# Performance work log

Hardware: AMD Instinct MI355X
Metric: run time of the kernel (lower is better)

## Reference

```python
import jax, jax.numpy as jnp
import numpy as np

H = 256; NL = 6; N = 64; DCONV = 4; DIN = 512; HEADS = 8; P = 64
CONVD = DIN + 2 * N            # 640
PROJ = 2 * DIN + 2 * N + HEADS  # 1160


def rmsnorm(x, w, eps=1e-6):
    return x * jax.lax.rsqrt(jnp.mean(x * x, axis=-1, keepdims=True) + eps) * w


def mamba2(x, Win, conv_w, conv_b, dt_bias, A_log, D, gnorm, Wout):
    # x: (b, l, H)
    b, l, _ = x.shape
    zxbcdt = x @ Win                       # (b, l, PROJ)
    z = zxbcdt[..., :DIN]
    xBC = zxbcdt[..., DIN:DIN + CONVD]
    dt = zxbcdt[..., DIN + CONVD:]         # (b, l, HEADS)
    # causal depthwise conv1d along l
    xp = jnp.pad(xBC, ((0, 0), (DCONV - 1, 0), (0, 0)))
    xc = conv_b + sum(xp[:, k:k + l, :] * conv_w[k] for k in range(DCONV))
    xBC = jax.nn.silu(xc)
    xs = xBC[..., :DIN]
    B = xBC[..., DIN:DIN + N]
    C = xBC[..., DIN + N:]
    dt = jax.nn.softplus(dt + dt_bias)
    dA = jnp.exp(dt * (-jnp.exp(A_log)))   # (b, l, HEADS)
    xh = xs.reshape(b, l, HEADS, P)
    xdt = xh * dt[..., None]

    def step(h, inp):
        dA_t, xdt_t, B_t, C_t = inp
        h = dA_t[:, :, None, None] * h + xdt_t[..., None] * B_t[:, None, None, :]
        return h, jnp.einsum('bhpn,bn->bhp', h, C_t)

    h0 = jnp.zeros((b, HEADS, P, N), x.dtype)
    _, ys = jax.lax.scan(step, h0, (jnp.swapaxes(dA, 0, 1), jnp.swapaxes(xdt, 0, 1),
                                    jnp.swapaxes(B, 0, 1), jnp.swapaxes(C, 0, 1)))
    y = jnp.swapaxes(ys, 0, 1) + D[None, None, :, None] * xh   # (b, l, HEADS, P)
    y = y.reshape(b, l, DIN) * jax.nn.silu(z)
    return rmsnorm(y, gnorm) @ Wout


def dual_path(x, t_norm, t_Win, t_cw, t_cb, t_dtb, t_Alog, t_D, t_gn, t_Wout,
              b_norm, b_Win, b_cw, b_cb, b_dtb, b_Alog, b_D, b_gn, b_Wout):
    batch, time, bands, hdim = x.shape
    for i in range(NL):
        # time-axis pass (raw row-major reshape, matching torch .reshape semantics)
        xt = x.reshape(batch * bands, time, hdim)
        xt = xt + mamba2(rmsnorm(xt, t_norm[i]), t_Win[i], t_cw[i], t_cb[i],
                         t_dtb[i], t_Alog[i], t_D[i], t_gn[i], t_Wout[i])
        x = jnp.swapaxes(xt.reshape(batch, bands, time, hdim), 1, 2)
        # band-axis pass
        xb = x.reshape(batch * time, bands, hdim)
        xb = xb + mamba2(rmsnorm(xb, b_norm[i]), b_Win[i], b_cw[i], b_cb[i],
                         b_dtb[i], b_Alog[i], b_D[i], b_gn[i], b_Wout[i])
        x = xb.reshape(batch, time, bands, hdim)
    return x


def setup_inputs() -> dict:
    key = jax.random.key(0)
    ks = jax.random.split(key, 3)
    x = jax.random.normal(ks[0], (2, 512, 64, H), jnp.float32)

    def make_params(k):
        kk = jax.random.split(k, 5)
        g = lambda kx, sh, s: jax.random.normal(kx, sh, jnp.float32) * s
        return dict(
            norm=jnp.ones((NL, H), jnp.float32),
            Win=g(kk[0], (NL, H, PROJ), H ** -0.5),
            cw=g(kk[1], (NL, DCONV, CONVD), 0.2),
            cb=jnp.zeros((NL, CONVD), jnp.float32),
            dtb=g(kk[2], (NL, HEADS), 0.5),
            Alog=jnp.log(jnp.abs(g(kk[3], (NL, HEADS), 1.0)) + 0.5),
            D=jnp.ones((NL, HEADS), jnp.float32),
            gn=jnp.ones((NL, DIN), jnp.float32),
            Wout=g(kk[4], (NL, DIN, H), DIN ** -0.5),
        )

    tp = make_params(ks[1]); bp = make_params(ks[2])
    out = {'x': x}
    for name, d in (('t', tp), ('b', bp)):
        for kname, v in d.items():
            out[f'{name}_{kname}'] = v
    return out


def reference(x, t_norm, t_Win, t_cw, t_cb, t_dtb, t_Alog, t_D, t_gn, t_Wout,
              b_norm, b_Win, b_cw, b_cb, b_dtb, b_Alog, b_D, b_gn, b_Wout):
    return dual_path(x, t_norm, t_Win, t_cw, t_cb, t_dtb, t_Alog, t_D, t_gn, t_Wout,
                     b_norm, b_Win, b_cw, b_cb, b_dtb, b_Alog, b_D, b_gn, b_Wout)
```

## Files before the change

### kernel.cpp

```cpp
#include <hip/hip_runtime.h>
#include <math.h>

#define NLAY   6
#define Hd     256
#define DINv   512
#define NHEADS 8
#define CONVDv 640
#define PROJv  1160
#define ZW     656
#define NTOK   65536
#define NCH    1024

typedef __attribute__((ext_vector_type(8))) short bf16x8;
typedef __attribute__((ext_vector_type(4))) float f32x4;
typedef unsigned short u16;

__device__ __forceinline__ float siluf(float v) { return v / (1.0f + expf(-v)); }
__device__ __forceinline__ float bflo(unsigned u) { return __uint_as_float(u << 16); }
__device__ __forceinline__ float bfhi(unsigned u) { return __uint_as_float(u & 0xffff0000u); }
__device__ __forceinline__ u16 f2b(float f) {
    unsigned u = __float_as_uint(f);
    return (u16)((u + 0x7fffu + ((u >> 16) & 1u)) >> 16);
}
__device__ __forceinline__ float b2f(u16 s) { return __uint_as_float(((unsigned)s) << 16); }

__device__ __forceinline__ void gl_lds16(const void* g, void* l) {
    __builtin_amdgcn_global_load_lds((const __attribute__((address_space(1))) unsigned int*)g,
                                     (__attribute__((address_space(3))) unsigned int*)l, 16, 0, 0);
}

__global__ __launch_bounds__(512)
void kprep_win(const float* __restrict__ tW, const float* __restrict__ bW,
               u16* __restrict__ Whi, u16* __restrict__ Wlo)
{
    const int li = blockIdx.y, j = blockIdx.x;
    const int t  = threadIdx.x;
    const int kk = t >> 6, col = (t >> 2) & 15, quad = t & 3;
    const float* W = (li < 6) ? (tW + (size_t)li * Hd * PROJv)
                              : (bW + (size_t)(li - 6) * Hd * PROJv);
    const int fullcol = 16 * j + col;
    const size_t ob = ((size_t)li * 74 + j) * 4096 + kk * 512 + col * 32 + quad * 8;
#pragma unroll
    for (int e = 0; e < 8; e++) {
        const int k = kk * 32 + quad * 8 + e;
        const float v = (fullcol < PROJv) ? W[(size_t)k * PROJv + fullcol] : 0.f;
        const u16 hi = f2b(v);
        Whi[ob + e] = hi;
        Wlo[ob + e] = f2b(v - b2f(hi));
    }
}

__global__ __launch_bounds__(512)
void kprep_wout(const float* __restrict__ tW, const float* __restrict__ tg,
                const float* __restrict__ bW, const float* __restrict__ bg,
                u16* __restrict__ Whi, u16* __restrict__ Wlo)
{
    const int li = blockIdx.y, j = blockIdx.x;
    const int t  = threadIdx.x;
    const int kk = t >> 5, col = (t >> 1) & 15, qh = t & 1;
    const float* W = (li < 6) ? tW + (size_t)li * DINv * Hd : bW + (size_t)(li - 6) * DINv * Hd;
    const float* g = (li < 6) ? tg + li * DINv : bg + (li - 6) * DINv;
    const int fullcol = 16 * j + col;
#pragma unroll
    for (int q = 0; q < 2; q++) {
        const int quad = qh * 2 + q;
        const size_t ob = ((size_t)li * 16 + j) * 8192 + kk * 512 + col * 32 + quad * 8;
#pragma unroll
        for (int e = 0; e < 8; e++) {
            const int k = kk * 32 + quad * 8 + e;
            const float v = W[(size_t)k * Hd + fullcol] * g[k];
            const u16 hi = f2b(v);
            Whi[ob + e] = hi;
            Wlo[ob + e] = f2b(v - b2f(hi));
        }
    }
}

__global__ __launch_bounds__(512, 4)
void k1_mfma(const float* __restrict__ src, u16* __restrict__ zs,
             u16* __restrict__ xrawT, u16* __restrict__ bnd,
             const float* __restrict__ nw,
             const u16* __restrict__ Whi, const u16* __restrict__ Wlo)
{
    __shared__ __align__(16) char smem[67584];
    u16* sAh = (u16*)smem;
    u16* sAl = sAh + 64 * 264;
    const int tid = threadIdx.x;
    const int cb  = blockIdx.x;
    const int R0  = cb * 64;

    {
        const int tok = tid >> 3, l8 = tid & 7;
        const float* xr = src + ((size_t)(R0 + tok)) * Hd + l8 * 32;
        float vv[32];
#pragma unroll
        for (int q = 0; q < 8; q++) {
            float4 v = ((const float4*)xr)[q];
            vv[4*q] = v.x; vv[4*q+1] = v.y; vv[4*q+2] = v.z; vv[4*q+3] = v.w;
        }
        float ss = 0.f;
#pragma unroll
        for (int j = 0; j < 32; j++) ss += vv[j] * vv[j];
#pragma unroll
        for (int m = 4; m >= 1; m >>= 1) ss += __shfl_xor(ss, m, 8);
        const float rstd = rsqrtf(ss * (1.0f / Hd) + 1e-6f);
        const float* nr = nw + l8 * 32;
        u16* dh = sAh + tok * 264 + l8 * 32;
        u16* dl = sAl + tok * 264 + l8 * 32;
#pragma unroll
        for (int j = 0; j < 32; j++) {
            const float val = vv[j] * rstd * nr[j];
            const u16 hi = f2b(val);
            dh[j] = hi;
            dl[j] = f2b(val - b2f(hi));
        }
    }
    __syncthreads();

    const int lane = tid & 63, wave = tid >> 6;
    const int rh = wave >> 1, cw = wave & 1;
    const int quad = lane >> 4, m16 = lane & 15;

    bf16x8 ah[8], al[8];
    {
        const u16* ph = sAh + (rh * 16 + m16) * 264 + quad * 8;
        const u16* pl = sAl + (rh * 16 + m16) * 264 + quad * 8;
#pragma unroll
        for (int kk = 0; kk < 8; kk++) {
            ah[kk] = *(const bf16x8*)(ph + kk * 32);
            al[kk] = *(const bf16x8*)(pl + kk * 32);
        }
    }
    __syncthreads();

    u16* sW = (u16*)smem;

#define K1_STAGE(p, buf)                                                          \
    {                                                                             \
        const int obase = wave * 4096;                                            \
        _Pragma("unroll")                                                         \
        for (int i = 0; i < 4; i++) {                                             \
            const int o = obase + i * 1024;                                       \
            const int chunk = o >> 13, t2 = chunk >> 1, hl = chunk & 1;           \
            const int within = o & 8191;                                          \
            const u16* sbase = (hl ? Wlo : Whi) + (size_t)(2 * (p) + t2) * 4096;  \
            gl_lds16((const char*)sbase + within + lane * 16,                     \
                     (char*)sW + (buf) * 32768 + o);                              \
        }                                                                         \
    }

    K1_STAGE(0, 0);
    __syncthreads();

    for (int p = 0; p < 37; p++) {
        if (p < 36) K1_STAGE(p + 1, (p + 1) & 1);
        const int j = 2 * p + cw;
        const u16* tb = sW + (p & 1) * 16384 + cw * 8192 + m16 * 32 + quad * 8;
        f32x4 acc = (f32x4){0.f, 0.f, 0.f, 0.f};
#pragma unroll
        for (int kk = 0; kk < 8; kk++) {
            bf16x8 bh = *(const bf16x8*)(tb + kk * 512);
            bf16x8 bl = *(const bf16x8*)(tb + 4096 + kk * 512);
            acc = __builtin_amdgcn_mfma_f32_16x16x32_bf16(ah[kk], bh, acc, 0, 0, 0);
            acc = __builtin_amdgcn_mfma_f32_16x16x32_bf16(al[kk], bh, acc, 0, 0, 0);
            acc = __builtin_amdgcn_mfma_f32_16x16x32_bf16(ah[kk], bl, acc, 0, 0, 0);
        }
        const int fullcol = 16 * j + m16;
        if (j < 32) {
            u16* zr = zs + (size_t)(R0 + rh * 16 + quad * 4) * ZW + fullcol;
#pragma unroll
            for (int i = 0; i < 4; i++) zr[(size_t)i * ZW] = f2b(acc[i]);
        } else if (j < 64) {
            const int ch = fullcol - 512;
            uint2 v;
            v.x = (unsigned)f2b(acc[0]) | ((unsigned)f2b(acc[1]) << 16);
            v.y = (unsigned)f2b(acc[2]) | ((unsigned)f2b(acc[3]) << 16);
            *(uint2*)(xrawT + ((size_t)cb * 512 + ch) * 64 + rh * 16 + quad * 4) = v;
            if (rh == 3 && quad == 3) {
#pragma unroll
                for (int i = 1; i < 4; i++)
                    bnd[((size_t)cb * 3 + (i - 1)) * 640 + ch] = f2b(acc[i]);
            }
        } else if (j < 73) {
            const int zc = fullcol - 512;
            u16* zr = zs + (size_t)(R0 + rh * 16 + quad * 4) * ZW + zc;
#pragma unroll
            for (int i = 0; i < 4; i++) zr[(size_t)i * ZW] = f2b(acc[i]);
            if (j < 72 && rh == 3 && quad == 3) {
#pragma unroll
                for (int i = 1; i < 4; i++)
                    bnd[((size_t)cb * 3 + (i - 1)) * 640 + zc] = f2b(acc[i]);
            }
        }
        __syncthreads();
    }
#undef K1_STAGE
}

__global__ __launch_bounds__(256, 4)
void k2a_conv(u16* __restrict__ zs, u16* __restrict__ xrawT,
              float* __restrict__ spb, const u16* __restrict__ bnd,
              const float* __restrict__ cwp, const float* __restrict__ cbp,
              const float* __restrict__ dtbp, const float* __restrict__ alogp, int L)
{
    const int tid = threadIdx.x;
    const int cb  = blockIdx.x;
    const size_t row0 = (size_t)cb * 64;
    const bool atStart = (((int)(row0 % (size_t)L)) == 0);

#pragma unroll
    for (int cc = 0; cc < 2; cc++) {
        const int ch = tid + cc * 256;
        const float w0 = cwp[0*CONVDv + ch], w1 = cwp[1*CONVDv + ch],
                    w2 = cwp[2*CONVDv + ch], w3 = cwp[3*CONVDv + ch];
        const float bias = cbp[ch];
        float h1 = 0.f, h2 = 0.f, h3 = 0.f;
        if (!atStart) {
            const u16* bp = bnd + ((size_t)(cb - 1) * 3) * 640 + ch;
            h3 = b2f(bp[0]);
            h2 = b2f(bp[640]);
            h1 = b2f(bp[1280]);
        }
        u16* xp = xrawT + ((size_t)cb * 512 + ch) * 64;
#pragma unroll
        for (int seg = 0; seg < 4; seg++) {
            uint4 a = ((const uint4*)xp)[seg * 2];
            uint4 b = ((const uint4*)xp)[seg * 2 + 1];
            unsigned uu[8] = {a.x, a.y, a.z, a.w, b.x, b.y, b.z, b.w};
            float in[16];
#pragma unroll
            for (int k = 0; k < 8; k++) { in[2*k] = bflo(uu[k]); in[2*k+1] = bfhi(uu[k]); }
            u16 o[16];
#pragma unroll
            for (int t = 0; t < 16; t++) {
                const float xv = in[t];
                o[t] = f2b(siluf(bias + w0*h3 + w1*h2 + w2*h1 + w3*xv));
                h3 = h2; h2 = h1; h1 = xv;
            }
            uint4 oa, ob;
            oa.x = o[0] | ((unsigned)o[1] << 16);   oa.y = o[2] | ((unsigned)o[3] << 16);
            oa.z = o[4] | ((unsigned)o[5] << 16);   oa.w = o[6] | ((unsigned)o[7] << 16);
            ob.x = o[8] | ((unsigned)o[9] << 16);   ob.y = o[10] | ((unsigned)o[11] << 16);
            ob.z = o[12] | ((unsigned)o[13] << 16); ob.w = o[14] | ((unsigned)o[15] << 16);
            ((uint4*)xp)[seg * 2] = oa;
            ((uint4*)xp)[seg * 2 + 1] = ob;
        }
    }

    if (tid < 128) {
        const int ch = 512 + tid;
        const float w0 = cwp[0*CONVDv + ch], w1 = cwp[1*CONVDv + ch],
                    w2 = cwp[2*CONVDv + ch], w3 = cwp[3*CONVDv + ch];
        const float bias = cbp[ch];
        float h1 = 0.f, h2 = 0.f, h3 = 0.f;
        if (!atStart) {
            const u16* bp = bnd + ((size_t)(cb - 1) * 3) * 640 + ch;
            h3 = b2f(bp[0]); h2 = b2f(bp[640]); h1 = b2f(bp[1280]);
        }
        u16* zp = zs + row0 * ZW + ch;
        for (int t = 0; t < 64; t++) {
            const float xv = b2f(zp[(size_t)t * ZW]);
            zp[(size_t)t * ZW] = f2b(siluf(bias + w0*h3 + w1*h2 + w2*h1 + w3*xv));
            h3 = h2; h2 = h1; h1 = xv;
        }
    }

    if (tid < NHEADS) {
        const float dtb = dtbp[tid], nA = -expf(alogp[tid]);
        const u16* dp = zs + row0 * ZW + 640 + tid;
        for (int t = 0; t < 64; t++) {
            const float dts = b2f(dp[(size_t)t * ZW]) + dtb;
            const float sp = (dts > 20.f) ? dts : log1pf(expf(dts));
            spb[(row0 + t) * 24 + tid] = sp;
            spb[(row0 + t) * 24 + 8 + tid] = nA * sp;
        }
    }
}

template<bool TMODE>
__global__ __launch_bounds__(256, 3)
void k2b_ssd(u16* __restrict__ zs, u16* __restrict__ xrawT,
             float* __restrict__ spb, u16* __restrict__ Sbuf,
             const float* __restrict__ Dp)
{
    __shared__ __align__(16) float sG[64][68];
    __shared__ float sClog[NHEADS][64];
    __shared__ float sSp[NHEADS][64];
    __shared__ float sWd[NHEADS][64];
    __shared__ __align__(16) u16 sBT[64][72];
    const int tid = threadIdx.x;
    const int lane = tid & 63, wave = tid >> 6;
    const int quad = lane >> 4, m16 = lane & 15;
    const int cb = blockIdx.x;
    const size_t row0 = (size_t)cb * 64;

    if (TMODE) {
        const int t_ = tid >> 2, ns = (tid & 3) * 16;
        const u16* br = zs + (row0 + t_) * ZW + 512 + ns;
        uint4 a = ((const uint4*)br)[0], b = ((const uint4*)br)[1];
        unsigned uu[8] = {a.x, a.y, a.z, a.w, b.x, b.y, b.z, b.w};
#pragma unroll
        for (int k = 0; k < 8; k++) {
            sBT[ns + 2*k][t_]     = (u16)(uu[k] & 0xffff);
            sBT[ns + 2*k + 1][t_] = (u16)(uu[k] >> 16);
        }
    }

    {
        const u16* cp = zs + (row0 + 16 * wave + m16) * ZW + 576 + quad * 8;
        bf16x8 cf0 = *(const bf16x8*)(cp);
        bf16x8 cf1 = *(const bf16x8*)(cp + 32);
#pragma unroll
        for (int st = 0; st < 4; st++) {
            const u16* bp = zs + (row0 + 16 * st + m16) * ZW + 512 + quad * 8;
            f32x4 acc = (f32x4){0.f, 0.f, 0.f, 0.f};
            acc = __builtin_amdgcn_mfma_f32_16x16x32_bf16(cf0, *(const bf16x8*)(bp), acc, 0, 0, 0);
            acc = __builtin_amdgcn_mfma_f32_16x16x32_bf16(cf1, *(const bf16x8*)(bp + 32), acc, 0, 0, 0);
#pragma unroll
            for (int i = 0; i < 4; i++)
                sG[16 * wave + quad * 4 + i][16 * st + m16] = acc[i];
        }
    }

#pragma unroll
    for (int hh = 0; hh < 2; hh++) {
        const int h = wave * 2 + hh;
        float c = spb[(row0 + lane) * 24 + 8 + h];
        const float sp = spb[(row0 + lane) * 24 + h];
#pragma unroll
        for (int d = 1; d < 64; d <<= 1) {
            const float o = __shfl_up(c, d, 64);
            if (lane >= d) c += o;
        }
        sClog[h][lane] = c;
        sSp[h][lane] = sp;
        if (TMODE) {
            spb[(row0 + lane) * 24 + 16 + h] = __expf(c);
            const float cl63 = __shfl(c, 63, 64);
            sWd[h][lane] = __expf(cl63 - c) * sp;
        }
    }
    __syncthreads();

    if (TMODE) {
        for (int h = 0; h < NHEADS; h++) {
            bf16x8 Ahi[2], Alo[2];
#pragma unroll
            for (int kk = 0; kk < 2; kk++) {
                const u16* xp = xrawT + ((size_t)cb * 512 + h * 64 + 16 * wave + m16) * 64
                                + 32 * kk + quad * 8;
                bf16x8 xf = *(const bf16x8*)xp;
                const float* wp = &sWd[h][32 * kk + quad * 8];
#pragma unroll
                for (int j = 0; j < 8; j++) {
                    const float v = b2f((u16)xf[j]) * wp[j];
                    const u16 hi = f2b(v);
                    Ahi[kk][j] = (short)hi;
                    Alo[kk][j] = (short)f2b(v - b2f(hi));
                }
            }
            u16* sb = Sbuf + ((size_t)cb * 8 + h) * 4096;
#pragma unroll
            for (int nt = 0; nt < 4; nt++) {
                f32x4 acc = (f32x4){0.f, 0.f, 0.f, 0.f};
#pragma unroll
                for (int kk = 0; kk < 2; kk++) {
                    const bf16x8 bf_ = *(const bf16x8*)(&sBT[16 * nt + m16][32 * kk + quad * 8]);
                    acc = __builtin_amdgcn_mfma_f32_16x16x32_bf16(Ahi[kk], bf_, acc, 0, 0, 0);
                    acc = __builtin_amdgcn_mfma_f32_16x16x32_bf16(Alo[kk], bf_, acc, 0, 0, 0);
                }
#pragma unroll
                for (int i = 0; i < 4; i++)
                    sb[(16 * wave + quad * 4 + i) * 64 + 16 * nt + m16] = f2b(acc[i]);
            }
        }
        __syncthreads();
    }

    const int t = 16 * wave + m16;
    for (int h = 0; h < NHEADS; h++) {
        const float Dh = Dp[h];
        const float clt = sClog[h][t];
        bf16x8 Mhi[2], Mlo[2];
#pragma unroll
        for (int kk = 0; kk < 2; kk++) {
            const float* gp = &sG[t][32 * kk + quad * 8];
            const float* cp = &sClog[h][32 * kk + quad * 8];
            const float* pp = &sSp[h][32 * kk + quad * 8];
#pragma unroll
            for (int j = 0; j < 8; j++) {
                const int s = 32 * kk + quad * 8 + j;
                float m = (s <= t) ? (__expf(clt - cp[j]) * pp[j] * gp[j]) : 0.f;
                if (s == t) m += Dh;
                const u16 hi = f2b(m);
                Mhi[kk][j] = (short)hi;
                Mlo[kk][j] = (short)f2b(m - b2f(hi));
            }
        }
        bf16x8 xf[4][2];
#pragma unroll
        for (int pt = 0; pt < 4; pt++)
#pragma unroll
            for (int kk = 0; kk < 2; kk++)
                xf[pt][kk] = *(const bf16x8*)(xrawT
                    + ((size_t)cb * 512 + h * 64 + 16 * pt + m16) * 64 + 32 * kk + quad * 8);
        if (TMODE) __syncthreads();
        f32x4 accY[4];
#pragma unroll
        for (int pt = 0; pt < 4; pt++) {
            accY[pt] = (f32x4){0.f, 0.f, 0.f, 0.f};
#pragma unroll
            for (int kk = 0; kk < 2; kk++) {
                accY[pt] = __builtin_amdgcn_mfma_f32_16x16x32_bf16(Mhi[kk], xf[pt][kk], accY[pt], 0, 0, 0);
                accY[pt] = __builtin_amdgcn_mfma_f32_16x16x32_bf16(Mlo[kk], xf[pt][kk], accY[pt], 0, 0, 0);
            }
        }
#pragma unroll
        for (int pt = 0; pt < 4; pt++) {
            if (TMODE) {
                uint2 v;
                v.x = (unsigned)f2b(accY[pt][0]) | ((unsigned)f2b(accY[pt][1]) << 16);
                v.y = (unsigned)f2b(accY[pt][2]) | ((unsigned)f2b(accY[pt][3]) << 16);
                *(uint2*)(xrawT + ((size_t)cb * 512 + h * 64 + 16 * pt + m16) * 64
                          + 16 * wave + quad * 4) = v;
            } else {
#pragma unroll
                for (int i = 0; i < 4; i++) {
                    const size_t row = row0 + 16 * wave + quad * 4 + i;
                    const int col = h * 64 + 16 * pt + m16;
                    const u16 zv = zs[row * ZW + col];
                    zs[row * ZW + col] = f2b(accY[pt][i] * siluf(b2f(zv)));
                }
            }
        }
    }
}

__global__ __launch_bounds__(64, 4)
void k2c_states(u16* __restrict__ Sbuf, const float* __restrict__ spb)
{
    const int p = threadIdx.x, h = blockIdx.y, s = blockIdx.x;
    float H[64];
#pragma unroll
    for (int n = 0; n < 64; n++) H[n] = 0.f;
    for (int c = 1; c < 8; c++) {
        const float P = spb[((size_t)s * 512 + (c - 1) * 64 + 63) * 24 + 16 + h];
        u16* sp_ = Sbuf + (((size_t)(s * 8 + c - 1) * 8 + h) * 4096) + p * 64;
#pragma unroll
        for (int n = 0; n < 64; n += 8) {
            uint4 v = *(const uint4*)(sp_ + n);
            unsigned uu[4] = {v.x, v.y, v.z, v.w};
            float sv[8];
#pragma unroll
            for (int w2 = 0; w2 < 4; w2++) { sv[2*w2] = bflo(uu[w2]); sv[2*w2+1] = bfhi(uu[w2]); }
#pragma unroll
            for (int e = 0; e < 8; e++) H[n + e] = fmaf(P, H[n + e], sv[e]);
            uint4 o;
            o.x = (unsigned)f2b(H[n+0]) | ((unsigned)f2b(H[n+1]) << 16);
            o.y = (unsigned)f2b(H[n+2]) | ((unsigned)f2b(H[n+3]) << 16);
            o.z = (unsigned)f2b(H[n+4]) | ((unsigned)f2b(H[n+5]) << 16);
            o.w = (unsigned)f2b(H[n+6]) | ((unsigned)f2b(H[n+7]) << 16);
            *(uint4*)(sp_ + n) = o;
        }
    }
}

__global__ __launch_bounds__(256, 4)
void k2d_corr(u16* __restrict__ zs, const u16* __restrict__ xrawT,
              const float* __restrict__ spb, const u16* __restrict__ Sbuf)
{
    const int tid = threadIdx.x;
    const int lane = tid & 63, wave = tid >> 6;
    const int quad = lane >> 4, m16 = lane & 15;
    const int cb = blockIdx.x;
    const int c = cb & 7;
    const size_t row0 = (size_t)cb * 64;

    for (int h = 0; h < NHEADS; h++) {
        f32x4 acc[4];
#pragma unroll
        for (int pt = 0; pt < 4; pt++) {
            const uint2 v = *(const uint2*)(xrawT
                + ((size_t)cb * 512 + h * 64 + 16 * pt + m16) * 64 + 16 * wave + quad * 4);
            acc[pt][0] = bflo(v.x); acc[pt][1] = bfhi(v.x);
            acc[pt][2] = bflo(v.y); acc[pt][3] = bfhi(v.y);
        }
        if (c) {
            const float at = spb[(row0 + 16 * wave + m16) * 24 + 16 + h];
            bf16x8 Ahi[2], Alo[2];
#pragma unroll
            for (int kk = 0; kk < 2; kk++) {
                const u16* cp = zs + (row0 + 16 * wave + m16) * ZW + 576 + 32 * kk + quad * 8;
                bf16x8 cf = *(const bf16x8*)cp;
#pragma unroll
                for (int j = 0; j < 8; j++) {
                    const float v = b2f((u16)cf[j]) * at;
                    const u16 hi = f2b(v);
                    Ahi[kk][j] = (short)hi;
                    Alo[kk][j] = (short)f2b(v - b2f(hi));
                }
            }
            const u16* hb = Sbuf + ((size_t)(cb - 1) * 8 + h) * 4096;
#pragma unroll
            for (int pt = 0; pt < 4; pt++) {
#pragma unroll
                for (int kk = 0; kk < 2; kk++) {
                    bf16x8 hf = *(const bf16x8*)(hb + (16 * pt + m16) * 64 + 32 * kk + quad * 8);
                    acc[pt] = __builtin_amdgcn_mfma_f32_16x16x32_bf16(Ahi[kk], hf, acc[pt], 0, 0, 0);
                    acc[pt] = __builtin_amdgcn_mfma_f32_16x16x32_bf16(Alo[kk], hf, acc[pt], 0, 0, 0);
                }
            }
        }
#pragma unroll
        for (int pt = 0; pt < 4; pt++) {
#pragma unroll
            for (int i = 0; i < 4; i++) {
                const size_t row = row0 + 16 * wave + quad * 4 + i;
                const int col = h * 64 + 16 * pt + m16;
                const u16 zv = zs[row * ZW + col];
                zs[row * ZW + col] = f2b(acc[pt][i] * siluf(b2f(zv)));
            }
        }
    }
}

template<bool TMODE>
__global__ __launch_bounds__(512, 2)
void k3_mfma(const u16* __restrict__ zs, const float* __restrict__ src,
             float* __restrict__ dst,
             const u16* __restrict__ Whi, const u16* __restrict__ Wlo)
{
    __shared__ __align__(16) char smem[66560];
    float* sAf = (float*)smem;
    const int tid = threadIdx.x;
    const int R0  = blockIdx.x * 128;
    const int lane = tid & 63, wave = tid >> 6;
    const int quad = lane >> 4, m16 = lane & 15;

    bf16x8 ah[16], al[16];

    for (int b = 0; b < 4; b++) {
        {
            const int tok = tid >> 4, l16 = tid & 15;
            const u16* yr = zs + (size_t)(R0 + b * 32 + tok) * ZW + l16 * 32;
            float v[32];
#pragma unroll
            for (int q = 0; q < 4; q++) {
                uint4 u = ((const uint4*)yr)[q];
                unsigned uu[4] = {u.x, u.y, u.z, u.w};
#pragma unroll
                for (int w2 = 0; w2 < 4; w2++) {
                    v[8*q + 2*w2]     = bflo(uu[w2]);
                    v[8*q + 2*w2 + 1] = bfhi(uu[w2]);
                }
            }
            float ss = 0.f;
#pragma unroll
            for (int j = 0; j < 32; j++) ss += v[j] * v[j];
#pragma unroll
            for (int m = 8; m >= 1; m >>= 1) ss += __shfl_xor(ss, m, 16);
            const float rstd = rsqrtf(ss * (1.0f / DINv) + 1e-6f);
            float* dp = sAf + tok * 516 + l16 * 32;
#pragma unroll
            for (int j = 0; j < 32; j++) dp[j] = v[j] * rstd;
        }
        __syncthreads();
        if ((wave >> 1) == b) {
            const int r = (wave & 1) * 16 + m16;
            const float* fp = sAf + r * 516 + quad * 8;
#pragma unroll
            for (int kk = 0; kk < 16; kk++) {
                float4 fa = ((const float4*)(fp + kk * 32))[0];
                float4 fb = ((const float4*)(fp + kk * 32))[1];
                float f[8] = {fa.x, fa.y, fa.z, fa.w, fb.x, fb.y, fb.z, fb.w};
                bf16x8 hv, lv;
#pragma unroll
                for (int e = 0; e < 8; e++) {
                    const u16 hi = f2b(f[e]);
                    hv[e] = (short)hi;
                    lv[e] = (short)f2b(f[e] - b2f(hi));
                }
                ah[kk] = hv;
                al[kk] = lv;
            }
        }
        __syncthreads();
    }

    f32x4 acc[16];
#pragma unroll
    for (int j = 0; j < 16; j++) acc[j] = (f32x4){0.f, 0.f, 0.f, 0.f};

#define K3_STAGE(j, buf)                                                          \
    {                                                                             \
        const int obase = wave * 4096;                                            \
        _Pragma("unroll")                                                         \
        for (int i = 0; i < 4; i++) {                                             \
            const int o = obase + i * 1024;                                       \
            const char* gsrc = (o < 16384)                                        \
                ? ((const char*)(Whi + (size_t)(j) * 8192) + o)                   \
                : ((const char*)(Wlo + (size_t)(j) * 8192) + (o - 16384));        \
            gl_lds16(gsrc + lane * 16, smem + (buf) * 32768 + o);                 \
        }                                                                         \
    }

    K3_STAGE(0, 0);
    __syncthreads();

    for (int j = 0; j < 16; j++) {
        if (j < 15) K3_STAGE(j + 1, (j + 1) & 1);
        const u16* tb = (const u16*)(smem + (j & 1) * 32768) + m16 * 32 + quad * 8;
#pragma unroll
        for (int kk = 0; kk < 16; kk++) {
            bf16x8 bh = *(const bf16x8*)(tb + kk * 512);
            bf16x8 bl = *(const bf16x8*)(tb + 8192 + kk * 512);
            acc[j] = __builtin_amdgcn_mfma_f32_16x16x32_bf16(ah[kk], bh, acc[j], 0, 0, 0);
            acc[j] = __builtin_amdgcn_mfma_f32_16x16x32_bf16(al[kk], bh, acc[j], 0, 0, 0);
            acc[j] = __builtin_amdgcn_mfma_f32_16x16x32_bf16(ah[kk], bl, acc[j], 0, 0, 0);
        }
        __syncthreads();
    }
#undef K3_STAGE

#pragma unroll
    for (int j = 0; j < 16; j++) {
        const int col = 16 * j + m16;
#pragma unroll
        for (int i = 0; i < 4; i++) {
            const size_t inrow = (size_t)(R0 + wave * 16 + quad * 4 + i);
            const float v = acc[j][i] + src[inrow * Hd + col];
            size_t orow;
            if (TMODE) {
                const size_t sq = inrow >> 9;
                const size_t tt = inrow & 511;
                orow = ((sq >> 6) * 512 + tt) * 64 + (sq & 63);
            } else {
                orow = inrow;
            }
            dst[orow * Hd + col] = v;
        }
    }
}

extern "C" void kernel_launch(void* const* d_in, const int* in_sizes, int n_in,
                              void* d_out, int out_size, void* d_ws, size_t ws_size,
                              hipStream_t stream) {
    const float* x      = (const float*)d_in[0];
    const float* t_norm = (const float*)d_in[1];
    const float* t_Win  = (const float*)d_in[2];
    const float* t_cw   = (const float*)d_in[3];
    const float* t_cb   = (const float*)d_in[4];
    const float* t_dtb  = (const float*)d_in[5];
    const float* t_Alog = (const float*)d_in[6];
    const float* t_D    = (const float*)d_in[7];
    const float* t_gn   = (const float*)d_in[8];
    const float* t_Wout = (const float*)d_in[9];
    const float* b_norm = (const float*)d_in[10];
    const float* b_Win  = (const float*)d_in[11];
    const float* b_cw   = (const float*)d_in[12];
    const float* b_cb   = (const float*)d_in[13];
    const float* b_dtb  = (const float*)d_in[14];
    const float* b_Alog = (const float*)d_in[15];
    const float* b_D    = (const float*)d_in[16];
    const float* b_gn   = (const float*)d_in[17];
    const float* b_Wout = (const float*)d_in[18];

    float* out = (float*)d_out;
    char*  wsb = (char*)d_ws;
    float* xbuf = (float*)wsb;
    u16*   Sbuf = (u16*)wsb;
    size_t off = 67108864;
    u16* W1hi = (u16*)(wsb + off); off += (size_t)12 * 74 * 4096 * 2;
    u16* W1lo = (u16*)(wsb + off); off += (size_t)12 * 74 * 4096 * 2;
    u16* W2hi = (u16*)(wsb + off); off += (size_t)12 * 16 * 8192 * 2;
    u16* W2lo = (u16*)(wsb + off); off += (size_t)12 * 16 * 8192 * 2;
    u16* zs   = (u16*)(wsb + off); off += (size_t)NTOK * ZW * 2;
    float* spb = (float*)(wsb + off); off += (size_t)NTOK * 24 * 4;
    u16* xrawT = (u16*)(wsb + off); off += (size_t)NTOK * 512 * 2;
    u16* bnd  = (u16*)(wsb + off);

    kprep_win<<<dim3(74, 12), 512, 0, stream>>>(t_Win, b_Win, W1hi, W1lo);
    kprep_wout<<<dim3(16, 12), 512, 0, stream>>>(t_Wout, t_gn, b_Wout, b_gn, W2hi, W2lo);

    for (int i = 0; i < NLAY; i++) {
        const float* src_t = (i == 0) ? x : out;
        k1_mfma<<<NCH, 512, 0, stream>>>(src_t, zs, xrawT, bnd, t_norm + i * Hd,
                 W1hi + (size_t)i * 74 * 4096, W1lo + (size_t)i * 74 * 4096);
        k2a_conv<<<NCH, 256, 0, stream>>>(zs, xrawT, spb, bnd,
                 t_cw + i * 4 * CONVDv, t_cb + i * CONVDv, t_dtb + i * NHEADS,
                 t_Alog + i * NHEADS, 512);
        k2b_ssd<true><<<NCH, 256, 0, stream>>>(zs, xrawT, spb, Sbuf, t_D + i * NHEADS);
        k2c_states<<<dim3(128, NHEADS), 64, 0, stream>>>(Sbuf, spb);
        k2d_corr<<<NCH, 256, 0, stream>>>(zs, xrawT, spb, Sbuf);
        k3_mfma<true><<<NTOK/128, 512, 0, stream>>>(zs, src_t, xbuf,
                 W2hi + (size_t)i * 16 * 8192, W2lo + (size_t)i * 16 * 8192);
        k1_mfma<<<NCH, 512, 0, stream>>>(xbuf, zs, xrawT, bnd, b_norm + i * Hd,
                 W1hi + (size_t)(i + 6) * 74 * 4096, W1lo + (size_t)(i + 6) * 74 * 4096);
        k2a_conv<<<NCH, 256, 0, stream>>>(zs, xrawT, spb, bnd,
                 b_cw + i * 4 * CONVDv, b_cb + i * CONVDv, b_dtb + i * NHEADS,
                 b_Alog + i * NHEADS, 64);
        k2b_ssd<false><<<NCH, 256, 0, stream>>>(zs, xrawT, spb, Sbuf, b_D + i * NHEADS);
        k3_mfma<false><<<NTOK/128, 512, 0, stream>>>(zs, xbuf, out,
                 W2hi + (size_t)(i + 6) * 16 * 8192, W2lo + (size_t)(i + 6) * 16 * 8192);
    }
}
```

Baseline: 6.259 ms.

## Parallelize conv kernel: split sequence halves, stage B/C via LDS, vectorize dt

Reworks the depthwise conv kernel so each xs channel's 64-step sequence is processed as two 32-step halves. The second half is done first, using the three preceding raw values as history, and is written in place. The B/C channels are staged into shared memory through async global-to-LDS loads, convolved with two threads per channel, and written back as coalesced rows, replacing strided per-element global accesses. The dt softplus is spread over 64 threads with vector stores instead of 8 threads looping, and silu uses fast exp and reciprocal, which slightly changes numerics.

```diff
diff --git a/kernel.cpp b/kernel.cpp
--- a/kernel.cpp
+++ b/kernel.cpp
@@ -15,7 +15,9 @@
 typedef __attribute__((ext_vector_type(4))) float f32x4;
 typedef unsigned short u16;
 
-__device__ __forceinline__ float siluf(float v) { return v / (1.0f + expf(-v)); }
+__device__ __forceinline__ float siluf(float v) {
+    return v * __builtin_amdgcn_rcpf(1.0f + __expf(-v));
+}
 __device__ __forceinline__ float bflo(unsigned u) { return __uint_as_float(u << 16); }
 __device__ __forceinline__ float bfhi(unsigned u) { return __uint_as_float(u & 0xffff0000u); }
 __device__ __forceinline__ u16 f2b(float f) {
@@ -197,83 +199,128 @@
 #undef K1_STAGE
 }
 
+__device__ __forceinline__ void conv32_rmw(u16* xp, float w0, float w1, float w2, float w3,
+                                           float bias, float h3, float h2, float h1)
+{
+    uint4 va = ((const uint4*)xp)[0], vb = ((const uint4*)xp)[1],
+          vc = ((const uint4*)xp)[2], vd = ((const uint4*)xp)[3];
+    unsigned uu[16] = {va.x, va.y, va.z, va.w, vb.x, vb.y, vb.z, vb.w,
+                       vc.x, vc.y, vc.z, vc.w, vd.x, vd.y, vd.z, vd.w};
+    unsigned ou[16];
+#pragma unroll
+    for (int k = 0; k < 16; k++) {
+        const float x0 = bflo(uu[k]);
+        const u16 o0 = f2b(siluf(bias + w0*h3 + w1*h2 + w2*h1 + w3*x0));
+        h3 = h2; h2 = h1; h1 = x0;
+        const float x1 = bfhi(uu[k]);
+        const u16 o1 = f2b(siluf(bias + w0*h3 + w1*h2 + w2*h1 + w3*x1));
+        h3 = h2; h2 = h1; h1 = x1;
+        ou[k] = (unsigned)o0 | ((unsigned)o1 << 16);
+    }
+    ((uint4*)xp)[0] = make_uint4(ou[0],  ou[1],  ou[2],  ou[3]);
+    ((uint4*)xp)[1] = make_uint4(ou[4],  ou[5],  ou[6],  ou[7]);
+    ((uint4*)xp)[2] = make_uint4(ou[8],  ou[9],  ou[10], ou[11]);
+    ((uint4*)xp)[3] = make_uint4(ou[12], ou[13], ou[14], ou[15]);
+}
+
 __global__ __launch_bounds__(256, 4)
 void k2a_conv(u16* __restrict__ zs, u16* __restrict__ xrawT,
               float* __restrict__ spb, const u16* __restrict__ bnd,
               const float* __restrict__ cwp, const float* __restrict__ cbp,
               const float* __restrict__ dtbp, const float* __restrict__ alogp, int L)
 {
+    __shared__ __align__(16) u16 sBC[64][128];
     const int tid = threadIdx.x;
     const int cb  = blockIdx.x;
     const size_t row0 = (size_t)cb * 64;
     const bool atStart = (((int)(row0 % (size_t)L)) == 0);
+    const int lane = tid & 63, wave = tid >> 6;
+
+#pragma unroll
+    for (int j = 0; j < 4; j++) {
+        const int t0 = wave * 16 + j * 4;
+        gl_lds16(zs + (row0 + t0 + (lane >> 4)) * ZW + 512 + (lane & 15) * 8,
+                 (char*)sBC + t0 * 256);
+    }
 
 #pragma unroll
     for (int cc = 0; cc < 2; cc++) {
         const int ch = tid + cc * 256;
         const float w0 = cwp[0*CONVDv + ch], w1 = cwp[1*CONVDv + ch],
                     w2 = cwp[2*CONVDv + ch], w3 = cwp[3*CONVDv + ch];
-        const float bias = cbp[ch];
-        float h1 = 0.f, h2 = 0.f, h3 = 0.f;
-        if (!atStart) {
-            const u16* bp = bnd + ((size_t)(cb - 1) * 3) * 640 + ch;
-            h3 = b2f(bp[0]);
-            h2 = b2f(bp[640]);
-            h1 = b2f(bp[1280]);
-        }
-        u16* xp = xrawT + ((size_t)cb * 512 + ch) * 64;
-#pragma unroll
-        for (int seg = 0; seg < 4; seg++) {
-            uint4 a = ((const uint4*)xp)[seg * 2];
-            uint4 b = ((const uint4*)xp)[seg * 2 + 1];
-            unsigned uu[8] = {a.x, a.y, a.z, a.w, b.x, b.y, b.z, b.w};
-            float in[16];
-#pragma unroll
-            for (int k = 0; k < 8; k++) { in[2*k] = bflo(uu[k]); in[2*k+1] = bfhi(uu[k]); }
-            u16 o[16];
-#pragma unroll
-            for (int t = 0; t < 16; t++) {
-                const float xv = in[t];
-                o[t] = f2b(siluf(bias + w0*h3 + w1*h2 + w2*h1 + w3*xv));
-                h3 = h2; h2 = h1; h1 = xv;
-            }
-            uint4 oa, ob;
-            oa.x = o[0] | ((unsigned)o[1] << 16);   oa.y = o[2] | ((unsigned)o[3] << 16);
-            oa.z = o[4] | ((unsigned)o[5] << 16);   oa.w = o[6] | ((unsigned)o[7] << 16);
-            ob.x = o[8] | ((unsigned)o[9] << 16);   ob.y = o[10] | ((unsigned)o[11] << 16);
-            ob.z = o[12] | ((unsigned)o[13] << 16); ob.w = o[14] | ((unsigned)o[15] << 16);
-            ((uint4*)xp)[seg * 2] = oa;
-            ((uint4*)xp)[seg * 2 + 1] = ob;
-        }
-    }
-
-    if (tid < 128) {
-        const int ch = 512 + tid;
+        u16* xp = xrawT + ((size_t)cb * 512 + ch) * 64 + 32;
+        const uint2 hv = *(const uint2*)(xp - 4);
+        conv32_rmw(xp, w0, w1, w2, w3, cbp[ch], bfhi(hv.x), bflo(hv.y), bfhi(hv.y));
+    }
+
+    if (tid < 64) {
+        const int t = tid;
+        const uint4 dv = *(const uint4*)(zs + (row0 + t) * ZW + 640);
+        const unsigned uu[4] = {dv.x, dv.y, dv.z, dv.w};
+        float sp[8], ld[8];
+#pragma unroll
+        for (int h = 0; h < 8; h++) {
+            const float d = ((h & 1) ? bfhi(uu[h >> 1]) : bflo(uu[h >> 1])) + dtbp[h];
+            const float s = (d > 20.f) ? d : __logf(1.f + __expf(d));
+            sp[h] = s;
+            ld[h] = -__expf(alogp[h]) * s;
+        }
+        float* ob = spb + (row0 + t) * 24;
+        *(float4*)(ob)      = make_float4(sp[0], sp[1], sp[2], sp[3]);
+        *(float4*)(ob + 4)  = make_float4(sp[4], sp[5], sp[6], sp[7]);
+        *(float4*)(ob + 8)  = make_float4(ld[0], ld[1], ld[2], ld[3]);
+        *(float4*)(ob + 12) = make_float4(ld[4], ld[5], ld[6], ld[7]);
+    }
+    __syncthreads();
+
+#pragma unroll
+    for (int cc = 0; cc < 2; cc++) {
+        const int ch = tid + cc * 256;
         const float w0 = cwp[0*CONVDv + ch], w1 = cwp[1*CONVDv + ch],
                     w2 = cwp[2*CONVDv + ch], w3 = cwp[3*CONVDv + ch];
-        const float bias = cbp[ch];
         float h1 = 0.f, h2 = 0.f, h3 = 0.f;
         if (!atStart) {
             const u16* bp = bnd + ((size_t)(cb - 1) * 3) * 640 + ch;
             h3 = b2f(bp[0]); h2 = b2f(bp[640]); h1 = b2f(bp[1280]);
         }
-        u16* zp = zs + row0 * ZW + ch;
-        for (int t = 0; t < 64; t++) {
-            const float xv = b2f(zp[(size_t)t * ZW]);
-            zp[(size_t)t * ZW] = f2b(siluf(bias + w0*h3 + w1*h2 + w2*h1 + w3*xv));
+        conv32_rmw(xrawT + ((size_t)cb * 512 + ch) * 64, w0, w1, w2, w3, cbp[ch], h3, h2, h1);
+    }
+
+    u16 o[32];
+    {
+        const int ch  = tid & 127;
+        const int th  = tid >> 7;
+        const int t0  = th * 32;
+        const int gch = 512 + ch;
+        const float w0 = cwp[0*CONVDv + gch], w1 = cwp[1*CONVDv + gch],
+                    w2 = cwp[2*CONVDv + gch], w3 = cwp[3*CONVDv + gch];
+        const float bias = cbp[gch];
+        float h1, h2, h3;
+        if (th) {
+            h3 = b2f(sBC[29][ch]); h2 = b2f(sBC[30][ch]); h1 = b2f(sBC[31][ch]);
+        } else if (!atStart) {
+            const u16* bp = bnd + ((size_t)(cb - 1) * 3) * 640 + gch;
+            h3 = b2f(bp[0]); h2 = b2f(bp[640]); h1 = b2f(bp[1280]);
+        } else { h1 = h2 = h3 = 0.f; }
+#pragma unroll
+        for (int t = 0; t < 32; t++) {
+            const float xv = b2f(sBC[t0 + t][ch]);
+            o[t] = f2b(siluf(bias + w0*h3 + w1*h2 + w2*h1 + w3*xv));
             h3 = h2; h2 = h1; h1 = xv;
         }
     }
-
-    if (tid < NHEADS) {
-        const float dtb = dtbp[tid], nA = -expf(alogp[tid]);
-        const u16* dp = zs + row0 * ZW + 640 + tid;
-        for (int t = 0; t < 64; t++) {
-            const float dts = b2f(dp[(size_t)t * ZW]) + dtb;
-            const float sp = (dts > 20.f) ? dts : log1pf(expf(dts));
-            spb[(row0 + t) * 24 + tid] = sp;
-            spb[(row0 + t) * 24 + 8 + tid] = nA * sp;
-        }
+    __syncthreads();
+    {
+        const int ch = tid & 127, t0 = (tid >> 7) * 32;
+#pragma unroll
+        for (int t = 0; t < 32; t++) sBC[t0 + t][ch] = o[t];
+    }
+    __syncthreads();
+#pragma unroll
+    for (int i = 0; i < 4; i++) {
+        const int g = tid + i * 256;
+        const int t = g >> 4, s16 = g & 15;
+        *(uint4*)(zs + (row0 + t) * ZW + 512 + s16 * 8) = *(const uint4*)(&sBC[t][s16 * 8]);
     }
 }
 
```

Result: faster. 5.543 ms (-11.4%).
